# Kernel tuning notes

Hardware: AMD Instinct MI355X
Metric: run time of the kernel (lower is better)

## Reference

```python
import jax, jax.numpy as jnp
import numpy as np
from jax import lax

NUM_GROUP = 2048
INIT_DIST = 1.0e10


def setup_inputs() -> dict:
    key = jax.random.key(0)
    k1, k2 = jax.random.split(key)
    B, N = 32, 100000
    xyz = jax.random.normal(k1, (B, N, 3), dtype=jnp.float32)
    farthest_init = jax.random.randint(k2, (B,), 0, N, dtype=jnp.int64)
    return {"xyz": xyz, "farthest_init": farthest_init}


def reference(xyz, farthest_init):
    # xyz: [B, N, 3], farthest_init: [B] initial farthest indices
    B, N, _ = xyz.shape
    farthest0 = farthest_init.astype(jnp.int32)
    dist0 = jnp.full((B, N), INIT_DIST, dtype=xyz.dtype)

    def step(carry, _):
        distance, farthest = carry
        # gather current centroid per batch: [B, 1, 3]
        centroid = jnp.take_along_axis(xyz, farthest[:, None, None], axis=1)
        d = jnp.sum((xyz - centroid) ** 2, axis=-1)          # [B, N]
        distance = jnp.minimum(distance, d)                   # masked update
        new_farthest = jnp.argmax(distance, axis=-1).astype(jnp.int32)
        return (distance, new_farthest), farthest

    (_, _), cent_t = lax.scan(step, (dist0, farthest0), None, length=NUM_GROUP)
    centroids = cent_t.T                                      # [B, num_group]
    sampled = jnp.take_along_axis(xyz, centroids[:, :, None], axis=1)  # [B, num_group, 3]
    return sampled
```

## Files before the change

### kernel.cpp

```cpp
#include <hip/hip_runtime.h>

#pragma clang fp contract(off)

#define BATCH 32
#define NPTS 100000
#define NGROUP 2048
#define NBLK_PER_BATCH 8
#define NPB (NPTS / NBLK_PER_BATCH)
#define TPB 512
#define NPT 25
#define TAIL (NPB - (NPT - 1) * TPB)

typedef unsigned long long u64;
typedef unsigned int u32;

static_assert(NPB * NBLK_PER_BATCH == NPTS, "block split must be exact");
static_assert(NPT * TPB >= NPB, "per-thread capacity");

__device__ __forceinline__ float fsub_x(float a, float b) {
  float r; asm("v_sub_f32 %0, %1, %2" : "=v"(r) : "v"(a), "v"(b)); return r;
}
__device__ __forceinline__ float fmul_x(float a, float b) {
  float r; asm("v_mul_f32 %0, %1, %2" : "=v"(r) : "v"(a), "v"(b)); return r;
}
__device__ __forceinline__ float fma_x(float a, float b, float c) {
  float r; asm("v_fma_f32 %0, %1, %2, %3" : "=v"(r) : "v"(a), "v"(b), "v"(c)); return r;
}


__global__ __launch_bounds__(TPB, 2)
void fps_kernel(const float* __restrict__ xyz,
                const int* __restrict__ finit,
                float* __restrict__ out,
                u64* __restrict__ slots)
{
  const int blk  = blockIdx.x;
  const int b    = blk & (BATCH - 1);
  const int j    = blk >> 5;
  const int tid  = threadIdx.x;
  const int lane = tid & 63;
  const int wid  = tid >> 6;

  __shared__ float sval[TPB / 64];
  __shared__ int   sidx[TPB / 64];
  __shared__ int   s_win;

  const float* xb = xyz + (size_t)b * NPTS * 3;
  const int base = j * NPB;

  float px[NPT], py[NPT], pz[NPT], pd[NPT];
#pragma unroll
  for (int i = 0; i < NPT; ++i) {
    const bool valid = (i < NPT - 1) || (tid < TAIL);
    const int p  = valid ? (tid + i * TPB) : 0;
    const int gp = base + p;
    px[i] = xb[gp * 3 + 0];
    py[i] = xb[gp * 3 + 1];
    pz[i] = xb[gp * 3 + 2];
    pd[i] = valid ? 1.0e10f : -1.0f;
  }

  int cur = finit[b];

  float cx = xb[cur * 3 + 0], cy = xb[cur * 3 + 1], cz = xb[cur * 3 + 2];

  u64* batchSlots = slots + (size_t)b * NBLK_PER_BATCH * 2;

  for (int t = 0; t < NGROUP; ++t) {
    if (j == 0 && tid == 0) {
      float* o = out + ((size_t)b * NGROUP + t) * 3;
      o[0] = cx; o[1] = cy; o[2] = cz;
    }
    if (t == NGROUP - 1) break;

    float bestv = -1.0f;
    int   besti = 0x7fffffff;
#pragma unroll
    for (int i = 0; i < NPT; ++i) {
      const bool valid = (i < NPT - 1) || (tid < TAIL);
      const float dx = fsub_x(px[i], cx);
      const float dy = fsub_x(py[i], cy);
      const float dz = fsub_x(pz[i], cz);
      const float d  = fma_x(dz, dz, fma_x(dy, dy, fmul_x(dx, dx)));
      if (valid) {
        const float nd = fminf(pd[i], d);
        pd[i] = nd;
        if (nd > bestv) { bestv = nd; besti = base + tid + i * TPB; }
      }
    }

#pragma unroll
    for (int off = 32; off > 0; off >>= 1) {
      const float ov = __shfl_xor(bestv, off, 64);
      const int   oi = __shfl_xor(besti, off, 64);
      if (ov > bestv || (ov == bestv && oi < besti)) { bestv = ov; besti = oi; }
    }
    if (lane == 0) { sval[wid] = bestv; sidx[wid] = besti; }
    __syncthreads();

    if (wid == 0) {
      const int nw = TPB / 64;
      float v  = (lane < nw) ? sval[lane] : -1.0f;
      int   ix = (lane < nw) ? sidx[lane] : 0x7fffffff;
#pragma unroll
      for (int off = nw / 2; off > 0; off >>= 1) {
        const float ov = __shfl_xor(v, off, 64);
        const int   oi = __shfl_xor(ix, off, 64);
        if (ov > v || (ov == v && oi < ix)) { v = ov; ix = oi; }
      }

      if (lane == 0) {
        const u64 packed = ((u64)__float_as_uint(v) << 32)
                         | ((u64)(u32)(t & 0x7FFF) << 17)
                         | (u64)((~(u32)ix) & 0x1FFFFu);
        atomicExch(batchSlots + (size_t)j * 2 + (t & 1), packed);
      }
      u64 got = 0;
      const u32 want = (u32)(t & 0x7FFF);
      u64* rp = batchSlots + (size_t)lane * 2 + (t & 1);
      bool ok;
      do {
        got = (lane < NBLK_PER_BATCH) ? atomicAdd(rp, 0ull) : 0ull;
        ok  = (lane >= NBLK_PER_BATCH) || (((u32)(got >> 17) & 0x7FFFu) == want);
      } while (!__all(ok));

      u64 bp = (lane < NBLK_PER_BATCH) ? got : 0ull;
#pragma unroll
      for (int off = 4; off > 0; off >>= 1) {
        const u64 o = __shfl_xor(bp, off, 64);
        if (o > bp) bp = o;
      }
      if (lane == 0) s_win = (int)((~(u32)bp) & 0x1FFFFu);
    }
    __syncthreads();

    cur = s_win;
    cx = xb[cur * 3 + 0];
    cy = xb[cur * 3 + 1];
    cz = xb[cur * 3 + 2];
  }
}

extern "C" void kernel_launch(void* const* d_in, const int* in_sizes, int n_in,
                              void* d_out, int out_size, void* d_ws, size_t ws_size,
                              hipStream_t stream) {
  const float* xyz   = (const float*)d_in[0];
  const int*   finit = (const int*)d_in[1];
  float*       out   = (float*)d_out;
  u64*         slots = (u64*)d_ws;

  hipMemsetAsync(d_ws, 0xFF, (size_t)BATCH * NBLK_PER_BATCH * 2 * sizeof(u64),
                 stream);

  fps_kernel<<<dim3(BATCH * NBLK_PER_BATCH), dim3(TPB), 0, stream>>>(xyz, finit, out, slots);
}
```

Measured before the change: 5.359 ms.

## Replace block-level reduction with per-wave global slots and all-wave polling

Removes the two __syncthreads and the shared-memory cross-wave reduction each iteration. Every wave now packs its best value and index into a u64, publishes it to a per-wave global slot with a relaxed atomic store, and polls all 64 wave slots of the batch with atomic loads before doing a shuffle max. This cuts the block barrier and serial wave-0 handoff out of the critical path. In exchange, polling traffic on the shared slots grows eightfold. Every wave also loads the centroid itself.

```diff
diff --git a/kernel.cpp b/kernel.cpp
--- a/kernel.cpp
+++ b/kernel.cpp
@@ -10,6 +10,7 @@
 #define TPB 512
 #define NPT 25
 #define TAIL (NPB - (NPT - 1) * TPB)
+#define NWAVE 64
 
 typedef unsigned long long u64;
 typedef unsigned int u32;
@@ -27,7 +28,6 @@
   float r; asm("v_fma_f32 %0, %1, %2, %3" : "=v"(r) : "v"(a), "v"(b), "v"(c)); return r;
 }
 
-
 __global__ __launch_bounds__(TPB, 2)
 void fps_kernel(const float* __restrict__ xyz,
                 const int* __restrict__ finit,
@@ -40,10 +40,7 @@
   const int tid  = threadIdx.x;
   const int lane = tid & 63;
   const int wid  = tid >> 6;
-
-  __shared__ float sval[TPB / 64];
-  __shared__ int   sidx[TPB / 64];
-  __shared__ int   s_win;
+  const int gw   = j * 8 + wid;
 
   const float* xb = xyz + (size_t)b * NPTS * 3;
   const int base = j * NPB;
@@ -64,14 +61,16 @@
 
   float cx = xb[cur * 3 + 0], cy = xb[cur * 3 + 1], cz = xb[cur * 3 + 2];
 
-  u64* batchSlots = slots + (size_t)b * NBLK_PER_BATCH * 2;
+  u64* bs = slots + (size_t)b * 2 * NWAVE;
 
   for (int t = 0; t < NGROUP; ++t) {
-    if (j == 0 && tid == 0) {
-      float* o = out + ((size_t)b * NGROUP + t) * 3;
-      o[0] = cx; o[1] = cy; o[2] = cz;
+    if (t == NGROUP - 1) {
+      if (j == 0 && tid == 0) {
+        float* o = out + ((size_t)b * NGROUP + t) * 3;
+        o[0] = cx; o[1] = cy; o[2] = cz;
+      }
+      break;
     }
-    if (t == NGROUP - 1) break;
 
     float bestv = -1.0f;
     int   besti = 0x7fffffff;
@@ -89,52 +88,41 @@
       }
     }
 
+    const u32 tag = (u32)(t & 0x7FFF);
+    u64 pk = ((u64)__float_as_uint(bestv) << 32)
+           | ((u64)tag << 17)
+           | (u64)((~(u32)besti) & 0x1FFFFu);
 #pragma unroll
     for (int off = 32; off > 0; off >>= 1) {
-      const float ov = __shfl_xor(bestv, off, 64);
-      const int   oi = __shfl_xor(besti, off, 64);
-      if (ov > bestv || (ov == bestv && oi < besti)) { bestv = ov; besti = oi; }
+      const u64 o = __shfl_xor(pk, off, 64);
+      if (o > pk) pk = o;
     }
-    if (lane == 0) { sval[wid] = bestv; sidx[wid] = besti; }
-    __syncthreads();
 
-    if (wid == 0) {
-      const int nw = TPB / 64;
-      float v  = (lane < nw) ? sval[lane] : -1.0f;
-      int   ix = (lane < nw) ? sidx[lane] : 0x7fffffff;
+    const int par = t & 1;
+    u64* wave_slot = bs + (size_t)par * NWAVE + gw;
+    if (lane == 0) {
+      __hip_atomic_store(wave_slot, pk, __ATOMIC_RELAXED,
+                         __HIP_MEMORY_SCOPE_AGENT);
+    }
+
+    if (j == 0 && tid == 0) {
+      float* o = out + ((size_t)b * NGROUP + t) * 3;
+      o[0] = cx; o[1] = cy; o[2] = cz;
+    }
+
+    u64* rp = bs + (size_t)par * NWAVE + lane;
+    u64 got;
+    do {
+      got = __hip_atomic_load(rp, __ATOMIC_RELAXED, __HIP_MEMORY_SCOPE_AGENT);
+    } while (!__all(((u32)(got >> 17) & 0x7FFFu) == tag));
+
 #pragma unroll
-      for (int off = nw / 2; off > 0; off >>= 1) {
-        const float ov = __shfl_xor(v, off, 64);
-        const int   oi = __shfl_xor(ix, off, 64);
-        if (ov > v || (ov == v && oi < ix)) { v = ov; ix = oi; }
-      }
+    for (int off = 32; off > 0; off >>= 1) {
+      const u64 o = __shfl_xor(got, off, 64);
+      if (o > got) got = o;
+    }
+    cur = (int)((~(u32)got) & 0x1FFFFu);
 
-      if (lane == 0) {
-        const u64 packed = ((u64)__float_as_uint(v) << 32)
-                         | ((u64)(u32)(t & 0x7FFF) << 17)
-                         | (u64)((~(u32)ix) & 0x1FFFFu);
-        atomicExch(batchSlots + (size_t)j * 2 + (t & 1), packed);
-      }
-      u64 got = 0;
-      const u32 want = (u32)(t & 0x7FFF);
-      u64* rp = batchSlots + (size_t)lane * 2 + (t & 1);
-      bool ok;
-      do {
-        got = (lane < NBLK_PER_BATCH) ? atomicAdd(rp, 0ull) : 0ull;
-        ok  = (lane >= NBLK_PER_BATCH) || (((u32)(got >> 17) & 0x7FFFu) == want);
-      } while (!__all(ok));
-
-      u64 bp = (lane < NBLK_PER_BATCH) ? got : 0ull;
-#pragma unroll
-      for (int off = 4; off > 0; off >>= 1) {
-        const u64 o = __shfl_xor(bp, off, 64);
-        if (o > bp) bp = o;
-      }
-      if (lane == 0) s_win = (int)((~(u32)bp) & 0x1FFFFu);
-    }
-    __syncthreads();
-
-    cur = s_win;
     cx = xb[cur * 3 + 0];
     cy = xb[cur * 3 + 1];
     cz = xb[cur * 3 + 2];
@@ -149,8 +137,7 @@
   float*       out   = (float*)d_out;
   u64*         slots = (u64*)d_ws;
 
-  hipMemsetAsync(d_ws, 0xFF, (size_t)BATCH * NBLK_PER_BATCH * 2 * sizeof(u64),
-                 stream);
+  hipMemsetAsync(d_ws, 0xFF, (size_t)BATCH * 2 * NWAVE * sizeof(u64), stream);
 
   fps_kernel<<<dim3(BATCH * NBLK_PER_BATCH), dim3(TPB), 0, stream>>>(xyz, finit, out, slots);
 }
```

Result: slower. 13.84 ms (+158.2%).
